# Kernel optimization log

Measured on AMD Instinct MI355X. Metric: run time of the kernel, lower is better.

## Reference

```python
import jax, jax.numpy as jnp
import numpy as np


def _warp(x, flow):
    """Backward bilinear warp (grid_sample equivalent, zeros padding).

    x:    [B, C, H, W] feature frame
    flow: [B, 2, H, W] per-pixel motion vector (x, y) in pixels
    Samples x at (px + flow_x, py + flow_y) with bilinear interpolation;
    out-of-bounds samples contribute zero (padding_mode='zeros').
    """
    B, C, H, W = x.shape
    ys, xs = jnp.meshgrid(jnp.arange(H, dtype=x.dtype), jnp.arange(W, dtype=x.dtype), indexing='ij')
    gx = xs[None] + flow[:, 0]  # [B, H, W] sample x coords
    gy = ys[None] + flow[:, 1]  # [B, H, W] sample y coords
    x0 = jnp.floor(gx)
    y0 = jnp.floor(gy)
    wx = gx - x0
    wy = gy - y0
    flat = x.reshape(B, C, H * W)

    def corner(xi, yi, w):
        valid = (xi >= 0) & (xi <= W - 1) & (yi >= 0) & (yi <= H - 1)
        xc = jnp.clip(xi, 0, W - 1).astype(jnp.int32)
        yc = jnp.clip(yi, 0, H - 1).astype(jnp.int32)
        idx = (yc * W + xc).reshape(B, 1, H * W)
        v = jnp.take_along_axis(flat, idx, axis=2).reshape(B, C, H, W)
        return v * (w * valid.astype(x.dtype))[:, None]

    return (corner(x0, y0, (1.0 - wx) * (1.0 - wy))
            + corner(x0 + 1.0, y0, wx * (1.0 - wy))
            + corner(x0, y0 + 1.0, (1.0 - wx) * wy)
            + corner(x0 + 1.0, y0 + 1.0, wx * wy))


def setup_inputs() -> dict:
    key = jax.random.key(0)
    k1, k2 = jax.random.split(key)
    B, I, C, H, W = 2, 5, 16, 544, 960
    features = jax.random.normal(k1, (B, I, C, H, W), dtype=jnp.float32)
    mv = jax.random.normal(k2, (B, I, 2, H, W), dtype=jnp.float32) * 4.0  # ~4 px motion
    return {"features": features, "mv": mv}


def reference(features, mv):
    """Accumulative backward warp.

    Original torch loop: for i in 1..I-1: for j = i-1 .. 0:
        features[:, i] = warp(features[:, i], mv[:, j])
    i.e. frame i is sequentially warped by mv[i-1], mv[i-2], ..., mv[0].
    Equivalent vectorized form: for j = I-2 .. 0, warp all frames > j by
    mv[:, j] simultaneously (each frame still sees mv indices in descending
    order), removing the per-frame Python loop.
    """
    I = features.shape[1]
    warp_frames = jax.vmap(_warp, in_axes=(1, None), out_axes=1)  # over frame axis
    out = features
    for j in range(I - 2, -1, -1):
        warped = warp_frames(out[:, j + 1:], mv[:, j])  # [B, I-1-j, C, H, W]
        out = out.at[:, j + 1:].set(warped)
    return out
```

## Files before the change

kernel.cpp:

```cpp
#include <hip/hip_runtime.h>
#include <stdint.h>

namespace {
constexpr int Wd = 960, Hd = 544, Cd = 16, Id = 5, Bd = 2;
constexpr int HW = Hd * Wd;
constexpr long CHW = (long)Cd * HW;
constexpr long FRAME_BSTRIDE = (long)Id * CHW;
constexpr long FLOW_BSTRIDE  = (long)Id * 2 * HW;

constexpr int TSX = 64, TSY = 32;
constexpr int HALO = 12;
constexpr int TWX = TSX + 2 * HALO;
constexpr int TWY = TSY + 2 * HALO;
constexpr int NCHUNK = 20;
constexpr int TILE_F = NCHUNK * 256;
constexpr int GX = Wd / TSX;
constexpr int GY = Hd / TSY;
constexpr int NWG = GX * GY * Bd;
}

struct F2 { float x, y; };
struct Job { const void* s; long ss; void* d; long ds; const float* fl; int sBF, dBF; };

__device__ __forceinline__ uint f2bf_bits(float v) {
  uint x = __float_as_uint(v);
  return (x + 0x7FFFu + ((x >> 16) & 1u)) >> 16;
}

#define DECODE_TILE()                                                        \
  const int orig = blockIdx.x;                                               \
  const int xcd  = orig & 7;                                                 \
  constexpr int q = NWG / 8, r = NWG % 8;                                    \
  const int wgid = (xcd < r ? xcd * (q + 1) : r * (q + 1) + (xcd - r) * q)   \
                 + (orig >> 3);                                              \
  const int b   = wgid / (GX * GY);                                          \
  const int rem = wgid - b * (GX * GY);                                      \
  const int tyb = rem / GX;                                                  \
  const int txb = rem - tyb * GX;                                            \
  const int X0 = txb * TSX;                                                  \
  const int Y0 = tyb * TSY;                                                  \
  const int t   = threadIdx.x;                                               \
  const int x   = X0 + ((t & 15) << 2);                                      \
  const int y   = Y0 + (t >> 4);                                             \
  const int pix = y * Wd + x;

#define PRECOMPUTE_WEIGHTS()                                                 \
  float4 fxv = *reinterpret_cast<const float4*>(fl + pix);                   \
  float4 fyv = *reinterpret_cast<const float4*>(fl + HW + pix);              \
  float w00[4], w10[4], w01[4], w11[4];                                      \
  int lA[4]; uint32_t pxy[4]; int fbm = 0;                                   \
  _Pragma("unroll")                                                          \
  for (int j = 0; j < 4; ++j) {                                              \
    float fx = (j==0)?fxv.x:(j==1)?fxv.y:(j==2)?fxv.z:fxv.w;                 \
    float fy = (j==0)?fyv.x:(j==1)?fyv.y:(j==2)?fyv.z:fyv.w;                 \
    float gx = (float)(x + j) + fx;                                          \
    float gy = (float)y + fy;                                                \
    float x0f = floorf(gx), y0f = floorf(gy);                                \
    float wx = gx - x0f, wy = gy - y0f;                                      \
    bool vx0 = (x0f >= 0.f) && (x0f <= (float)(Wd - 1));                     \
    bool vx1 = (x0f + 1.f >= 0.f) && (x0f + 1.f <= (float)(Wd - 1));         \
    bool vy0 = (y0f >= 0.f) && (y0f <= (float)(Hd - 1));                     \
    bool vy1 = (y0f + 1.f >= 0.f) && (y0f + 1.f <= (float)(Hd - 1));         \
    w00[j] = (1.f-wx)*(1.f-wy) * ((vx0 && vy0) ? 1.f : 0.f);                 \
    w10[j] = wx*(1.f-wy)       * ((vx1 && vy0) ? 1.f : 0.f);                 \
    w01[j] = (1.f-wx)*wy       * ((vx0 && vy1) ? 1.f : 0.f);                 \
    w11[j] = wx*wy             * ((vx1 && vy1) ? 1.f : 0.f);                 \
    int ix0 = (int)x0f;                                                      \
    int iy0 = (int)y0f;                                                      \
    int lx = ix0 - (X0 - HALO);                                              \
    int ly = iy0 - (Y0 - HALO);                                              \
    bool ft = (lx >= 0) & (lx <= TWX - 2) & (ly >= 0) & (ly <= TWY - 2);     \
    if (!ft) fbm |= (1 << j);                                                \
    int lxc = min(max(lx, 0), TWX - 2), lyc = min(max(ly, 0), TWY - 2);      \
    lA[j] = (lyc * TWX + lxc) * 4;                                           \
    uint32_t px_ = (uint32_t)min(max(ix0 + 128, 0), 65535);                  \
    uint32_t py_ = (uint32_t)min(max(iy0 + 128, 0), 65535);                  \
    pxy[j] = px_ | (py_ << 16);                                              \
  }

#define PRECOMPUTE_GOFF()                                                    \
  const int lane = t & 63;                                                   \
  const int wv   = t >> 6;                                                   \
  const int nck  = (wv < 4) ? 3 : 2;                                         \
  int goff[3];                                                               \
  _Pragma("unroll")                                                          \
  for (int k = 0; k < 3; ++k) {                                              \
    int ck = wv + 8 * k;                                                     \
    if (ck < NCHUNK) {                                                       \
      int foff = ck * 256 + lane * 4;                                        \
      int ly = foff / TWX;                                                   \
      int lx = foff - ly * TWX;                                              \
      int gxc = min(max(X0 - HALO + lx, 0), Wd - 4);                         \
      int gyc = min(max(Y0 - HALO + ly, 0), Hd - 1);                         \
      goff[k] = gyc * Wd + gxc;                                              \
    }                                                                        \
  }

#define WAITV(n3, n2)                                                        \
  if (wv < 4) { asm volatile("s_waitcnt vmcnt(" #n3 ")" ::: "memory"); }     \
  else        { asm volatile("s_waitcnt vmcnt(" #n2 ")" ::: "memory"); }

#define PHASE(c, n3, n2)                                                     \
  WAITV(n3, n2);                                                             \
  __builtin_amdgcn_s_barrier();                                              \
  __builtin_amdgcn_sched_barrier(0);                                         \
  if ((c) + 3 < Cd) fillq(((c) + 3) & 3, (c) + 3);                           \
  comp(c);

__global__ __launch_bounds__(512, 4) void warp_pipe(
    Job j0, Job j1, Job j2, Job j3, Job j4)
{
  __shared__ float tile[4 * TILE_F];

  const int jb = blockIdx.y;
  Job J = j0;
  if      (jb == 1) J = j1;
  else if (jb == 2) J = j2;
  else if (jb == 3) J = j3;
  else if (jb == 4) J = j4;

  DECODE_TILE();

  const float* sF32 = (const float*)J.s + (long)b * J.ss;
  float*       dF32 = (float*)J.d + (long)b * J.ds;
  uint16_t*    dB16 = (uint16_t*)J.d + (long)b * J.ds;
  const bool dBF = J.dBF != 0;

  if (J.fl == nullptr) {
#pragma unroll
    for (int c = 0; c < Cd; ++c)
      *reinterpret_cast<float4*>(dF32 + (long)c * HW + pix)
          = *reinterpret_cast<const float4*>(sF32 + (long)c * HW + pix);
    return;
  }

  const float* fl = J.fl + (long)b * FLOW_BSTRIDE;
  PRECOMPUTE_WEIGHTS();
  PRECOMPUTE_GOFF();

  auto fillq = [&](int buf, int c) {
    const float* sC = sF32 + (long)c * HW;
    float* base = &tile[buf * TILE_F];
#pragma unroll
    for (int k = 0; k < 3; ++k) {
      if (k < nck) {
        __builtin_amdgcn_global_load_lds(
            (__attribute__((address_space(1))) void*)(void*)(sC + goff[k]),
            (__attribute__((address_space(3))) void*)&base[(wv + 8 * k) * 256],
            16, 0, 0);
      }
    }
  };

  auto comp = [&](int c) {
    const float* tb = &tile[(c & 3) * TILE_F];
    float ov[4];
#pragma unroll
    for (int j = 0; j < 4; ++j) {
      F2 r0 = *(const F2*)((const char*)tb + lA[j]);
      F2 r1 = *(const F2*)((const char*)tb + lA[j] + TWX * 4);
      ov[j] = (w00[j] * r0.x + w10[j] * r0.y) + (w01[j] * r1.x + w11[j] * r1.y);
    }
    if (dBF) {
      uint p0 = f2bf_bits(ov[0]) | (f2bf_bits(ov[1]) << 16);
      uint p1 = f2bf_bits(ov[2]) | (f2bf_bits(ov[3]) << 16);
      *reinterpret_cast<uint2*>(dB16 + (long)c * HW + pix) = make_uint2(p0, p1);
    } else {
      *reinterpret_cast<float4*>(dF32 + (long)c * HW + pix)
          = make_float4(ov[0], ov[1], ov[2], ov[3]);
    }
  };

  fillq(0, 0); fillq(1, 1); fillq(2, 2);

  PHASE(0, 6, 4)  PHASE(1, 7, 5)  PHASE(2, 8, 6)
  PHASE(3, 9, 7)  PHASE(4, 9, 7)  PHASE(5, 9, 7)
  PHASE(6, 9, 7)  PHASE(7, 9, 7)  PHASE(8, 9, 7)
  PHASE(9, 9, 7)  PHASE(10, 9, 7) PHASE(11, 9, 7)
  PHASE(12, 9, 7) PHASE(13, 9, 7)
  PHASE(14, 6, 5) PHASE(15, 3, 3)

  if (fbm) {
    asm volatile("s_waitcnt vmcnt(0)" ::: "memory");
    for (int c = 0; c < Cd; ++c) {
      const float* sC = sF32 + (long)c * HW;
#pragma unroll
      for (int j = 0; j < 4; ++j) {
        if (fbm & (1 << j)) {
          uint32_t p = pxy[j];
          int ix0 = (int)(p & 0xffffu) - 128;
          int iy0 = (int)(p >> 16) - 128;
          int xc0 = min(max(ix0, 0), Wd - 1), xc1 = min(max(ix0 + 1, 0), Wd - 1);
          int yc0 = min(max(iy0, 0), Hd - 1), yc1 = min(max(iy0 + 1, 0), Hd - 1);
          float v = w00[j] * sC[yc0 * Wd + xc0] + w10[j] * sC[yc0 * Wd + xc1]
                  + w01[j] * sC[yc1 * Wd + xc0] + w11[j] * sC[yc1 * Wd + xc1];
          if (dBF) dB16[(long)c * HW + pix + j] = (uint16_t)f2bf_bits(v);
          else     dF32[(long)c * HW + pix + j] = v;
        }
      }
    }
  }
}

__global__ __launch_bounds__(512) void warp_bf16(
    Job j0, Job j1, Job j2, Job j3, Job j4)
{
  __shared__ float tile[2][TILE_F];

  const int jb = blockIdx.y;
  Job J = j0;
  if      (jb == 1) J = j1;
  else if (jb == 2) J = j2;
  else if (jb == 3) J = j3;
  else if (jb == 4) J = j4;

  DECODE_TILE();

  const uint16_t* sB16 = (const uint16_t*)J.s + (long)b * J.ss;
  float*          dF32 = (float*)J.d + (long)b * J.ds;
  uint16_t*       dB16 = (uint16_t*)J.d + (long)b * J.ds;
  const bool dBF = J.dBF != 0;

  const float* fl = J.fl + (long)b * FLOW_BSTRIDE;
  PRECOMPUTE_WEIGHTS();
  PRECOMPUTE_GOFF();

  uint2 ld[3];
  auto loadB = [&](int c) {
    const uint* gp = (const uint*)(sB16 + (long)c * HW);
#pragma unroll
    for (int k = 0; k < 3; ++k)
      if (k < nck) ld[k] = *(const uint2*)(gp + (goff[k] >> 1));
  };
  auto writeB = [&](int nb) {
#pragma unroll
    for (int k = 0; k < 3; ++k) {
      if (k < nck) {
        float4 f;
        f.x = __uint_as_float(ld[k].x << 16);
        f.y = __uint_as_float(ld[k].x & 0xFFFF0000u);
        f.z = __uint_as_float(ld[k].y << 16);
        f.w = __uint_as_float(ld[k].y & 0xFFFF0000u);
        *reinterpret_cast<float4*>(&tile[nb][(wv + 8 * k) * 256 + lane * 4]) = f;
      }
    }
  };

  loadB(0); writeB(0);

#pragma unroll
  for (int c = 0; c < Cd; ++c) {
    __syncthreads();
    const bool pre = (c + 1 < Cd);
    if (pre) loadB(c + 1);

    const float* tb = tile[c & 1];
    float ov[4];
#pragma unroll
    for (int j = 0; j < 4; ++j) {
      float v;
      if (!(fbm & (1 << j))) {
        F2 r0 = *(const F2*)((const char*)tb + lA[j]);
        F2 r1 = *(const F2*)((const char*)tb + lA[j] + TWX * 4);
        v = (w00[j] * r0.x + w10[j] * r0.y) + (w01[j] * r1.x + w11[j] * r1.y);
      } else {
        uint32_t p = pxy[j];
        int ix0 = (int)(p & 0xffffu) - 128;
        int iy0 = (int)(p >> 16) - 128;
        int xc0 = min(max(ix0, 0), Wd - 1), xc1 = min(max(ix0 + 1, 0), Wd - 1);
        int yc0 = min(max(iy0, 0), Hd - 1), yc1 = min(max(iy0 + 1, 0), Hd - 1);
        const uint16_t* su = sB16 + (long)c * HW;
        float v00 = __uint_as_float((uint)su[yc0 * Wd + xc0] << 16);
        float v10 = __uint_as_float((uint)su[yc0 * Wd + xc1] << 16);
        float v01 = __uint_as_float((uint)su[yc1 * Wd + xc0] << 16);
        float v11 = __uint_as_float((uint)su[yc1 * Wd + xc1] << 16);
        v = w00[j] * v00 + w10[j] * v10 + w01[j] * v01 + w11[j] * v11;
      }
      ov[j] = v;
    }
    if (dBF) {
      uint p0 = f2bf_bits(ov[0]) | (f2bf_bits(ov[1]) << 16);
      uint p1 = f2bf_bits(ov[2]) | (f2bf_bits(ov[3]) << 16);
      *reinterpret_cast<uint2*>(dB16 + (long)c * HW + pix) = make_uint2(p0, p1);
    } else {
      *reinterpret_cast<float4*>(dF32 + (long)c * HW + pix)
          = make_float4(ov[0], ov[1], ov[2], ov[3]);
    }
    if (pre) writeB((c + 1) & 1);
  }
}

extern "C" void kernel_launch(void* const* d_in, const int* in_sizes, int n_in,
                              void* d_out, int out_size, void* d_ws, size_t ws_size,
                              hipStream_t stream) {
  const float* feat = (const float*)d_in[0];
  const float* mv   = (const float*)d_in[1];
  float*       out  = (float*)d_out;

  dim3 block(512, 1, 1);
  const long FB = FRAME_BSTRIDE;
  auto mkjob = [](const void* s, long ss, void* d, long ds, const float* fl,
                  int sBF, int dBF) {
    Job j; j.s = s; j.ss = ss; j.d = d; j.ds = ds; j.fl = fl;
    j.sBF = sBF; j.dBF = dBF; return j;
  };
  Job Z = mkjob(nullptr, 0, nullptr, 0, nullptr, 0, 0);
  const float* flj[4] = { mv + 0L * 2 * HW, mv + 1L * 2 * HW,
                          mv + 2L * 2 * HW, mv + 3L * 2 * HW };

  auto launchP = [&](int nj, Job a, Job b, Job c, Job d, Job e) {
    warp_pipe<<<dim3(NWG, nj, 1), block, 0, stream>>>(a, b, c, d, e);
  };
  auto launchB = [&](int nj, Job a, Job b, Job c) {
    warp_bf16<<<dim3(NWG, nj, 1), block, 0, stream>>>(a, b, c, Z, Z);
  };

  const size_t need = (size_t)(4 * CHW) * Bd * sizeof(uint16_t);

  if (ws_size >= need) {
    uint16_t* W  = (uint16_t*)d_ws;
    const long WB = 4 * CHW;
    uint16_t* wa = W + 0 * CHW;
    uint16_t* wb = W + 1 * CHW;
    uint16_t* wd = W + 2 * CHW;
    uint16_t* wc = W + 3 * CHW;
    uint16_t* we = (uint16_t*)(out + 4 * CHW);
    const long EB = 2 * FB;

    launchP(5,
      mkjob(feat + 1 * CHW, FB, out + 1 * CHW, FB, flj[0], 0, 0),
      mkjob(feat + 2 * CHW, FB, wa, WB, flj[1], 0, 1),
      mkjob(feat + 3 * CHW, FB, wb, WB, flj[2], 0, 1),
      mkjob(feat + 4 * CHW, FB, wd, WB, flj[3], 0, 1),
      mkjob(feat, FB, out, FB, nullptr, 0, 0));
    launchB(3,
      mkjob(wa, WB, out + 2 * CHW, FB, flj[0], 1, 0),
      mkjob(wb, WB, wc, WB, flj[1], 1, 1),
      mkjob(wd, WB, we, EB, flj[2], 1, 1));
    launchB(2,
      mkjob(wc, WB, out + 3 * CHW, FB, flj[0], 1, 0),
      mkjob(we, EB, wa, WB, flj[1], 1, 1), Z);
    launchB(1, mkjob(wa, WB, out + 4 * CHW, FB, flj[0], 1, 0), Z, Z);
  } else {
    float* S = out;
    auto w1 = [&](const float* s, float* d, int j) {
      launchP(1, mkjob(s, FB, d, FB, flj[j], 0, 0), Z, Z, Z, Z);
    };
    w1(feat + 1 * CHW, out + 1 * CHW, 0);
    w1(feat + 2 * CHW, S, 1);
    w1(S, out + 2 * CHW, 0);
    w1(feat + 3 * CHW, out + 3 * CHW, 2);
    w1(out + 3 * CHW, S, 1);
    w1(S, out + 3 * CHW, 0);
    w1(feat + 4 * CHW, S, 3);
    w1(S, out + 4 * CHW, 2);
    w1(out + 4 * CHW, S, 1);
    w1(S, out + 4 * CHW, 0);
    launchP(1, mkjob(feat, FB, out, FB, nullptr, 0, 0), Z, Z, Z, Z);
  }
}
```

Measured before the change: 300.6 us.

## Pipeline bf16 warp kernel with async global-to-LDS loads and bf16 tiles

Replaces the double-buffered register-staged bf16 warp kernel with a 4-deep pipeline. It uses global_load_lds to copy bf16 tiles straight into shared memory, with a wider halo of 16, and keeps them as bf16 in LDS instead of widening to fp32. Out-of-tile samples are handled in a separate pass after the pipeline, so the main compute loop has no branch. This aims to hide load latency, cut LDS footprint so occupancy can rise, and remove register staging. The cost is per-element 16-bit LDS reads and a serialized fallback loop that rewrites some outputs.

```diff
diff --git a/kernel.cpp b/kernel.cpp
--- a/kernel.cpp
+++ b/kernel.cpp
@@ -9,11 +9,18 @@
 constexpr long FLOW_BSTRIDE  = (long)Id * 2 * HW;
 
 constexpr int TSX = 64, TSY = 32;
+
 constexpr int HALO = 12;
 constexpr int TWX = TSX + 2 * HALO;
 constexpr int TWY = TSY + 2 * HALO;
 constexpr int NCHUNK = 20;
 constexpr int TILE_F = NCHUNK * 256;
+
+constexpr int HB   = 16;
+constexpr int TWXB = TSX + 2 * HB;
+constexpr int TWYB = TSY + 2 * HB;
+constexpr int TILE_B = TWXB * TWYB;
+
 constexpr int GX = Wd / TSX;
 constexpr int GY = Hd / TSY;
 constexpr int NWG = GX * GY * Bd;
@@ -44,7 +51,7 @@
   const int y   = Y0 + (t >> 4);                                             \
   const int pix = y * Wd + x;
 
-#define PRECOMPUTE_WEIGHTS()                                                 \
+#define PRECOMPUTE_WEIGHTS(HALO_, TWX_, TWY_, SC_)                           \
   float4 fxv = *reinterpret_cast<const float4*>(fl + pix);                   \
   float4 fyv = *reinterpret_cast<const float4*>(fl + HW + pix);              \
   float w00[4], w10[4], w01[4], w11[4];                                      \
@@ -67,33 +74,15 @@
     w11[j] = wx*wy             * ((vx1 && vy1) ? 1.f : 0.f);                 \
     int ix0 = (int)x0f;                                                      \
     int iy0 = (int)y0f;                                                      \
-    int lx = ix0 - (X0 - HALO);                                              \
-    int ly = iy0 - (Y0 - HALO);                                              \
-    bool ft = (lx >= 0) & (lx <= TWX - 2) & (ly >= 0) & (ly <= TWY - 2);     \
+    int lx = ix0 - (X0 - (HALO_));                                           \
+    int ly = iy0 - (Y0 - (HALO_));                                           \
+    bool ft = (lx >= 0) & (lx <= (TWX_) - 2) & (ly >= 0) & (ly <= (TWY_) - 2);\
     if (!ft) fbm |= (1 << j);                                                \
-    int lxc = min(max(lx, 0), TWX - 2), lyc = min(max(ly, 0), TWY - 2);      \
-    lA[j] = (lyc * TWX + lxc) * 4;                                           \
+    int lxc = min(max(lx, 0), (TWX_) - 2), lyc = min(max(ly, 0), (TWY_) - 2);\
+    lA[j] = (lyc * (TWX_) + lxc) * (SC_);                                    \
     uint32_t px_ = (uint32_t)min(max(ix0 + 128, 0), 65535);                  \
     uint32_t py_ = (uint32_t)min(max(iy0 + 128, 0), 65535);                  \
     pxy[j] = px_ | (py_ << 16);                                              \
-  }
-
-#define PRECOMPUTE_GOFF()                                                    \
-  const int lane = t & 63;                                                   \
-  const int wv   = t >> 6;                                                   \
-  const int nck  = (wv < 4) ? 3 : 2;                                         \
-  int goff[3];                                                               \
-  _Pragma("unroll")                                                          \
-  for (int k = 0; k < 3; ++k) {                                              \
-    int ck = wv + 8 * k;                                                     \
-    if (ck < NCHUNK) {                                                       \
-      int foff = ck * 256 + lane * 4;                                        \
-      int ly = foff / TWX;                                                   \
-      int lx = foff - ly * TWX;                                              \
-      int gxc = min(max(X0 - HALO + lx, 0), Wd - 4);                         \
-      int gyc = min(max(Y0 - HALO + ly, 0), Hd - 1);                         \
-      goff[k] = gyc * Wd + gxc;                                              \
-    }                                                                        \
   }
 
 #define WAITV(n3, n2)                                                        \
@@ -135,8 +124,24 @@
   }
 
   const float* fl = J.fl + (long)b * FLOW_BSTRIDE;
-  PRECOMPUTE_WEIGHTS();
-  PRECOMPUTE_GOFF();
+  PRECOMPUTE_WEIGHTS(HALO, TWX, TWY, 4);
+
+  const int lane = t & 63;
+  const int wv   = t >> 6;
+  const int nck  = (wv < 4) ? 3 : 2;
+  int goff[3];
+#pragma unroll
+  for (int k = 0; k < 3; ++k) {
+    int ck = wv + 8 * k;
+    if (ck < NCHUNK) {
+      int foff = ck * 256 + lane * 4;
+      int ly = foff / TWX;
+      int lx = foff - ly * TWX;
+      int gxc = min(max(X0 - HALO + lx, 0), Wd - 4);
+      int gyc = min(max(Y0 - HALO + ly, 0), Hd - 1);
+      goff[k] = gyc * Wd + gxc;
+    }
+  }
 
   auto fillq = [&](int buf, int c) {
     const float* sC = sF32 + (long)c * HW;
@@ -202,17 +207,22 @@
   }
 }
 
-__global__ __launch_bounds__(512) void warp_bf16(
-    Job j0, Job j1, Job j2, Job j3, Job j4)
+#define BPH(c, n2, n1)                                                       \
+  if (wv < 4) { asm volatile("s_waitcnt vmcnt(" #n2 ")" ::: "memory"); }     \
+  else        { asm volatile("s_waitcnt vmcnt(" #n1 ")" ::: "memory"); }     \
+  __builtin_amdgcn_s_barrier();                                              \
+  __builtin_amdgcn_sched_barrier(0);                                         \
+  if ((c) + 3 < Cd) fillb(((c) + 3) & 3, (c) + 3);                           \
+  compb(c);
+
+__global__ __launch_bounds__(512, 4) void warp_bf16p(Job j0, Job j1, Job j2)
 {
-  __shared__ float tile[2][TILE_F];
+  __shared__ uint16_t tileB[4][TILE_B];
 
   const int jb = blockIdx.y;
   Job J = j0;
   if      (jb == 1) J = j1;
   else if (jb == 2) J = j2;
-  else if (jb == 3) J = j3;
-  else if (jb == 4) J = j4;
 
   DECODE_TILE();
 
@@ -222,61 +232,49 @@
   const bool dBF = J.dBF != 0;
 
   const float* fl = J.fl + (long)b * FLOW_BSTRIDE;
-  PRECOMPUTE_WEIGHTS();
-  PRECOMPUTE_GOFF();
-
-  uint2 ld[3];
-  auto loadB = [&](int c) {
-    const uint* gp = (const uint*)(sB16 + (long)c * HW);
-#pragma unroll
-    for (int k = 0; k < 3; ++k)
-      if (k < nck) ld[k] = *(const uint2*)(gp + (goff[k] >> 1));
-  };
-  auto writeB = [&](int nb) {
-#pragma unroll
-    for (int k = 0; k < 3; ++k) {
+  PRECOMPUTE_WEIGHTS(HB, TWXB, TWYB, 1);
+
+  const int lane = t & 63;
+  const int wv   = t >> 6;
+  const int nck  = (wv < 4) ? 2 : 1;
+  int goff[2];
+#pragma unroll
+  for (int k = 0; k < 2; ++k) {
+    int ck = wv + 8 * k;
+    if (ck < 12) {
+      int foff = ck * 512 + lane * 8;
+      int ly = foff / TWXB;
+      int lx = foff - ly * TWXB;
+      int gxc = min(max(X0 - HB + lx, 0), Wd - 8);
+      int gyc = min(max(Y0 - HB + ly, 0), Hd - 1);
+      goff[k] = gyc * Wd + gxc;
+    }
+  }
+
+  auto fillb = [&](int buf, int c) {
+    const uint16_t* sC = sB16 + (long)c * HW;
+#pragma unroll
+    for (int k = 0; k < 2; ++k) {
       if (k < nck) {
-        float4 f;
-        f.x = __uint_as_float(ld[k].x << 16);
-        f.y = __uint_as_float(ld[k].x & 0xFFFF0000u);
-        f.z = __uint_as_float(ld[k].y << 16);
-        f.w = __uint_as_float(ld[k].y & 0xFFFF0000u);
-        *reinterpret_cast<float4*>(&tile[nb][(wv + 8 * k) * 256 + lane * 4]) = f;
+        __builtin_amdgcn_global_load_lds(
+            (__attribute__((address_space(1))) void*)(void*)(sC + goff[k]),
+            (__attribute__((address_space(3))) void*)&tileB[buf][(wv + 8 * k) * 512],
+            16, 0, 0);
       }
     }
   };
 
-  loadB(0); writeB(0);
-
-#pragma unroll
-  for (int c = 0; c < Cd; ++c) {
-    __syncthreads();
-    const bool pre = (c + 1 < Cd);
-    if (pre) loadB(c + 1);
-
-    const float* tb = tile[c & 1];
+  auto compb = [&](int c) {
+    const uint16_t* tb = tileB[c & 3];
     float ov[4];
 #pragma unroll
     for (int j = 0; j < 4; ++j) {
-      float v;
-      if (!(fbm & (1 << j))) {
-        F2 r0 = *(const F2*)((const char*)tb + lA[j]);
-        F2 r1 = *(const F2*)((const char*)tb + lA[j] + TWX * 4);
-        v = (w00[j] * r0.x + w10[j] * r0.y) + (w01[j] * r1.x + w11[j] * r1.y);
-      } else {
-        uint32_t p = pxy[j];
-        int ix0 = (int)(p & 0xffffu) - 128;
-        int iy0 = (int)(p >> 16) - 128;
-        int xc0 = min(max(ix0, 0), Wd - 1), xc1 = min(max(ix0 + 1, 0), Wd - 1);
-        int yc0 = min(max(iy0, 0), Hd - 1), yc1 = min(max(iy0 + 1, 0), Hd - 1);
-        const uint16_t* su = sB16 + (long)c * HW;
-        float v00 = __uint_as_float((uint)su[yc0 * Wd + xc0] << 16);
-        float v10 = __uint_as_float((uint)su[yc0 * Wd + xc1] << 16);
-        float v01 = __uint_as_float((uint)su[yc1 * Wd + xc0] << 16);
-        float v11 = __uint_as_float((uint)su[yc1 * Wd + xc1] << 16);
-        v = w00[j] * v00 + w10[j] * v10 + w01[j] * v01 + w11[j] * v11;
-      }
-      ov[j] = v;
+      int ib = lA[j];
+      float v00 = __uint_as_float((uint)tb[ib]        << 16);
+      float v10 = __uint_as_float((uint)tb[ib + 1]    << 16);
+      float v01 = __uint_as_float((uint)tb[ib + TWXB] << 16);
+      float v11 = __uint_as_float((uint)tb[ib + TWXB + 1] << 16);
+      ov[j] = (w00[j] * v00 + w10[j] * v10) + (w01[j] * v01 + w11[j] * v11);
     }
     if (dBF) {
       uint p0 = f2bf_bits(ov[0]) | (f2bf_bits(ov[1]) << 16);
@@ -286,7 +284,39 @@
       *reinterpret_cast<float4*>(dF32 + (long)c * HW + pix)
           = make_float4(ov[0], ov[1], ov[2], ov[3]);
     }
-    if (pre) writeB((c + 1) & 1);
+  };
+
+  fillb(0, 0); fillb(1, 1); fillb(2, 2);
+
+  BPH(0, 4, 2)   BPH(1, 5, 3)   BPH(2, 6, 4)
+  BPH(3, 7, 5)   BPH(4, 7, 5)   BPH(5, 7, 5)
+  BPH(6, 7, 5)   BPH(7, 7, 5)   BPH(8, 7, 5)
+  BPH(9, 7, 5)   BPH(10, 7, 5)  BPH(11, 7, 5)
+  BPH(12, 7, 5)  BPH(13, 7, 5)
+  BPH(14, 5, 4)  BPH(15, 3, 3)
+
+  if (fbm) {
+    asm volatile("s_waitcnt vmcnt(0)" ::: "memory");
+    for (int c = 0; c < Cd; ++c) {
+      const uint16_t* su = sB16 + (long)c * HW;
+#pragma unroll
+      for (int j = 0; j < 4; ++j) {
+        if (fbm & (1 << j)) {
+          uint32_t p = pxy[j];
+          int ix0 = (int)(p & 0xffffu) - 128;
+          int iy0 = (int)(p >> 16) - 128;
+          int xc0 = min(max(ix0, 0), Wd - 1), xc1 = min(max(ix0 + 1, 0), Wd - 1);
+          int yc0 = min(max(iy0, 0), Hd - 1), yc1 = min(max(iy0 + 1, 0), Hd - 1);
+          float v00 = __uint_as_float((uint)su[yc0 * Wd + xc0] << 16);
+          float v10 = __uint_as_float((uint)su[yc0 * Wd + xc1] << 16);
+          float v01 = __uint_as_float((uint)su[yc1 * Wd + xc0] << 16);
+          float v11 = __uint_as_float((uint)su[yc1 * Wd + xc1] << 16);
+          float v = w00[j] * v00 + w10[j] * v10 + w01[j] * v01 + w11[j] * v11;
+          if (dBF) dB16[(long)c * HW + pix + j] = (uint16_t)f2bf_bits(v);
+          else     dF32[(long)c * HW + pix + j] = v;
+        }
+      }
+    }
   }
 }
 
@@ -312,7 +342,7 @@
     warp_pipe<<<dim3(NWG, nj, 1), block, 0, stream>>>(a, b, c, d, e);
   };
   auto launchB = [&](int nj, Job a, Job b, Job c) {
-    warp_bf16<<<dim3(NWG, nj, 1), block, 0, stream>>>(a, b, c, Z, Z);
+    warp_bf16p<<<dim3(NWG, nj, 1), block, 0, stream>>>(a, b, c);
   };
 
   const size_t need = (size_t)(4 * CHW) * Bd * sizeof(uint16_t);
```

New measurement: 511.2 us. 1.7x slower.
